# Kernel tuning notes

Hardware: AMD Instinct MI355X
Metric: run time of the kernel (lower is better)

The kernel has to match this reference:

```python
import jax, jax.numpy as jnp
import numpy as np

N = 1024      # params.input_dim (f1 is a square [N, N] similarity matrix)
TOPK = 16     # params.topk
B = 64        # hardcoded batch in the original reshape
W = 2 * N // B  # spatial width after reshape


def setup_inputs() -> dict:
    key = jax.random.key(0)
    k1, k2, k3 = jax.random.split(key, 3)
    f1 = jax.random.normal(k1, (N, N), dtype=jnp.float32)
    # Conv2d(in=N, out=N, kernel=(TOPK, 1)) weights, kaiming-ish scale
    conv_w = jax.random.normal(k2, (N, N, TOPK, 1), dtype=jnp.float32) * 0.01
    conv_b = jax.random.normal(k3, (N,), dtype=jnp.float32) * 0.01
    return {"f1": f1, "conv_w": conv_w, "conv_b": conv_b}


def reference(f1, conv_w, conv_b):
    # i = topk indices along last dim (largest, sorted) -> [N, TOPK]
    _, idx = jax.lax.top_k(f1, TOPK)
    # pos = f1[i]: gather rows of f1 by the topk column indices -> [N, TOPK, N]
    pos = f1[idx]
    # repeat_interleave(TOPK, dim=0).reshape(N, TOPK, -1) == each row tiled TOPK times
    rep = jnp.broadcast_to(f1[:, None, :], (N, TOPK, N))
    # cat on dim=2 -> [N, TOPK, 2N]; reshape to NCHW [B, N, TOPK, W]
    out = jnp.concatenate([rep, pos], axis=2).reshape(B, N, TOPK, W)
    # Conv2d kernel (TOPK, 1), VALID padding collapses H -> 1: [B, N, 1, W]
    y = jax.lax.conv_general_dilated(
        out, conv_w, window_strides=(1, 1), padding='VALID',
        dimension_numbers=('NCHW', 'OIHW', 'NCHW'))
    y = y + conv_b[None, :, None, None]
    return jax.nn.relu(y).reshape(N, -1)  # [N, B*W] = [N, 2N]
```

## Files before the change

### kernel.cpp

```cpp
#include <hip/hip_runtime.h>
#include <stdint.h>


#define NDIM 1024
#define TK   16
#define KPOS 8192
#define KREP 512
#define NCOL 2048

typedef unsigned short u16;
typedef uint32_t u32;
typedef u16   u16x8  __attribute__((ext_vector_type(8)));
typedef u32   u32x4  __attribute__((ext_vector_type(4)));
typedef __bf16 bf16x8 __attribute__((ext_vector_type(8)));
typedef float  f32x4  __attribute__((ext_vector_type(4)));

__device__ __forceinline__ u16 f2bf(float x) {
    union { float f; unsigned u; } v; v.f = x;
    unsigned r = 0x7FFFu + ((v.u >> 16) & 1u);
    return (u16)((v.u + r) >> 16);
}

__device__ __forceinline__ void load_lds_16B(const u16* g, u16* l) {
    __builtin_amdgcn_global_load_lds(
        (__attribute__((address_space(1))) void*)(uintptr_t)g,
        (__attribute__((address_space(3))) void*)(unsigned)(uintptr_t)l,
        16, 0, 0);
}

#define PREP_TOPK 256
#define PREP_ZERO 2048
#define PREP_CONV 4096
#define PREP_W1   1024

__global__ __launch_bounds__(256) void prep_kernel(const float* __restrict__ f1,
                                                   const float* __restrict__ W,
                                                   int* __restrict__ idx,
                                                   u16* __restrict__ Wb,
                                                   u16* __restrict__ W1b,
                                                   float* __restrict__ out) {
    const int bid = blockIdx.x;
    const int t = threadIdx.x;
    if (bid < PREP_TOPK) {
        const int lane = t & 63;
        const int row  = bid * 4 + (t >> 6);
        float v[16];
        const float* src = f1 + row * NDIM + lane;
        #pragma unroll
        for (int j = 0; j < 16; ++j) v[j] = src[j * 64];
        for (int sel = 0; sel < TK; ++sel) {
            float best = -3.402823466e38f; int bg = 0x7fffffff;
            #pragma unroll
            for (int j = 0; j < 16; ++j)
                if (v[j] > best) { best = v[j]; bg = j * 64 + lane; }
            #pragma unroll
            for (int s = 1; s < 64; s <<= 1) {
                float ov = __shfl_xor(best, s);
                int   og = __shfl_xor(bg, s);
                if (ov > best || (ov == best && og < bg)) { best = ov; bg = og; }
            }
            if (lane == sel) idx[row * TK + sel] = bg;
            #pragma unroll
            for (int j = 0; j < 16; ++j)
                if (bg == j * 64 + lane) v[j] = -3.402823466e38f;
        }
    } else if (bid < PREP_TOPK + PREP_ZERO) {
        const int zb = bid - PREP_TOPK;
        f32x4 z = {0.f, 0.f, 0.f, 0.f};
        *(f32x4*)(out + (size_t)(zb * 256 + t) * 4) = z;
    } else if (bid < PREP_TOPK + PREP_ZERO + PREP_CONV) {
        const int tid = (bid - PREP_TOPK - PREP_ZERO) * 256 + t;
        const int o  = tid >> 10;
        const int r  = tid & 1023;
        const int kp0 = r * 8;
        const int ip  = r >> 1;
        const int kh0 = (r & 1) * 8;
        const int i = (ip >> 5) * 64 + ((ip >> 1) & 15) * 4 + (ip & 1) + 2;
        const float* src = W + (size_t)o * 16384 + i * 16 + kh0;
        float4 a = *(const float4*)(src);
        float4 b = *(const float4*)(src + 4);
        u16x8 ov;
        ov[0] = f2bf(a.x); ov[1] = f2bf(a.y); ov[2] = f2bf(a.z); ov[3] = f2bf(a.w);
        ov[4] = f2bf(b.x); ov[5] = f2bf(b.y); ov[6] = f2bf(b.z); ov[7] = f2bf(b.w);
        *(u16x8*)(Wb + (size_t)o * KPOS + kp0) = ov;
    } else {
        const int o = bid - PREP_TOPK - PREP_ZERO - PREP_CONV;
        const float* wrow = W + (size_t)o * 16384;
        #pragma unroll
        for (int h = 0; h < 2; ++h) {
            const int kr = h * 256 + t;
            const int nl = kr >> 5, q = (kr >> 4) & 1, kh = kr & 15;
            const float* base = wrow + (nl * 64 + q) * 16 + kh;
            float s = 0.f;
            #pragma unroll
            for (int tt = 0; tt < 16; ++tt) s += base[tt * 64];
            W1b[o * KREP + kr] = f2bf(s);
        }
    }
}

__global__ __launch_bounds__(256) void buildx_kernel(const float* __restrict__ f1,
                                                     const int* __restrict__ idx,
                                                     u16* __restrict__ Xt,
                                                     u16* __restrict__ B1) {
    __shared__ u32 Ls[32 * 64];
    const int bid = blockIdx.x;
    const int t  = threadIdx.x;
    const int ci  = t >> 5;
    const int s   = t & 31;
    const int khp = s >> 2;
    const int wq  = s & 3;
    int b, i8, row, qoff, ostride;
    u16* dstbase;
    if (bid < 4096) {
        b = bid >> 6; i8 = bid & 63;
        const int ip = i8 * 8 + ci;
        const int nl = ip >> 5, tt = (ip >> 1) & 15, qp = ip & 1;
        row = idx[(b * 16 + nl) * TK + tt];
        qoff = qp * 512;
        dstbase = Xt; ostride = KPOS;
    } else {
        const int rb = bid - 4096;
        b = rb >> 2; i8 = rb & 3;
        const int iq = i8 * 8 + ci;
        row = b * 16 + (iq >> 1);
        qoff = (iq & 1) * 512;
        dstbase = B1; ostride = KREP;
    }
    const float* src = f1 + row * NDIM + qoff;
    const int base0 = khp * 64 + wq * 8;
    float4 a0 = *(const float4*)(src + base0);
    float4 a1 = *(const float4*)(src + base0 + 4);
    float4 b0 = *(const float4*)(src + base0 + 32);
    float4 b1 = *(const float4*)(src + base0 + 36);
    float lo[8] = {a0.x, a0.y, a0.z, a0.w, a1.x, a1.y, a1.z, a1.w};
    float hi[8] = {b0.x, b0.y, b0.z, b0.w, b1.x, b1.y, b1.z, b1.w};
    const int colsw = (ci * 8 + khp) ^ (wq << 3);
    #pragma unroll
    for (int j = 0; j < 8; ++j) {
        const int w = wq * 8 + j;
        u32 p = (u32)f2bf(lo[j]) | ((u32)f2bf(hi[j]) << 16);
        Ls[w * 64 + colsw] = p;
    }
    __syncthreads();
    const int wv = t >> 3, seg = t & 7;
    const int swz = wv & 24;
    u32x4 r0 = *(const u32x4*)(Ls + wv * 64 + ((seg * 8 + 0) ^ swz));
    u32x4 r1 = *(const u32x4*)(Ls + wv * 64 + ((seg * 8 + 4) ^ swz));
    u16* dst = dstbase + (size_t)(b * 32 + wv) * ostride + i8 * 128 + seg * 16;
    *(u32x4*)(dst)     = r0;
    *(u32x4*)(dst + 8) = r1;
}

#define BM 128
#define BN 128
#define BK 64

__global__ __launch_bounds__(256, 2) void gemm_kernel(const u16* __restrict__ Ap,
                                                      const u16* __restrict__ Bp,
                                                      const u16* __restrict__ A1,
                                                      const u16* __restrict__ B1,
                                                      float* __restrict__ out) {
    __shared__ __align__(16) u16 As[BM * BK];
    __shared__ __align__(16) u16 Bs[BN * BK];
    const int f = blockIdx.x;
    int m, n, kb, kiters, stride;
    const u16 *Ab, *Bb;
    if (f < 512) {
        m = f >> 6; const int u = f & 63; n = u & 15;
        stride = KPOS; kb = (u >> 4) * 2048; kiters = 32; Ab = Ap; Bb = Bp;
    } else {
        const int g = f - 512; m = g >> 4; n = g & 15;
        stride = KREP; kb = 0; kiters = 8; Ab = A1; Bb = B1;
    }
    const int t    = threadIdx.x;
    const int lane = t & 63;
    const int wave = t >> 6;
    const int wm   = (wave >> 1) * 64;
    const int wn   = (wave & 1) * 64;
    const int quad = lane >> 4;
    const int l16  = lane & 15;
    const int sw   = l16 & 7;
    const int o0 = m * BM;
    const int n0 = n * BN;

    f32x4 acc[4][4] = {};

    const int rA = t >> 3;
    const int c8 = t & 7;
    const int csw = (c8 ^ (rA & 7)) * 8;
    const u16* gA = Ab + (size_t)(o0 + rA) * stride + kb + csw;
    const u16* gB = Bb + (size_t)(n0 + rA) * stride + kb + csw;
    u16* lA = As + t * 8;
    u16* lB = Bs + t * 8;

    for (int it = 0; it < kiters; ++it) {
        const int k0 = it * BK;
        #pragma unroll
        for (int c = 0; c < 4; ++c) {
            load_lds_16B(gA + (size_t)(c * 32) * stride + k0, lA + c * 2048);
            load_lds_16B(gB + (size_t)(c * 32) * stride + k0, lB + c * 2048);
        }
        __syncthreads();

        #pragma unroll
        for (int ks = 0; ks < 2; ++ks) {
            bf16x8 af[4], bfr[4];
            #pragma unroll
            for (int mt = 0; mt < 4; ++mt) {
                u16x8 bits = *(const u16x8*)(As + (wm + mt * 16 + l16) * BK
                                                + (((ks * 4 + quad) ^ sw) * 8));
                af[mt] = __builtin_bit_cast(bf16x8, bits);
            }
            #pragma unroll
            for (int nt = 0; nt < 4; ++nt) {
                u16x8 bits = *(const u16x8*)(Bs + (wn + nt * 16 + l16) * BK
                                                + (((ks * 4 + quad) ^ sw) * 8));
                bfr[nt] = __builtin_bit_cast(bf16x8, bits);
            }
            #pragma unroll
            for (int mt = 0; mt < 4; ++mt)
                #pragma unroll
                for (int nt = 0; nt < 4; ++nt)
                    acc[mt][nt] = __builtin_amdgcn_mfma_f32_16x16x32_bf16(
                        af[mt], bfr[nt], acc[mt][nt], 0, 0, 0);
        }
        __syncthreads();
    }

    #pragma unroll
    for (int nt = 0; nt < 4; ++nt) {
        const int nn = n0 + wn + nt * 16 + l16;
        const int bb = nn >> 5, w = nn & 31;
        #pragma unroll
        for (int mt = 0; mt < 4; ++mt) {
            #pragma unroll
            for (int r = 0; r < 4; ++r) {
                const int o = o0 + wm + mt * 16 + quad * 4 + r;
                unsafeAtomicAdd(out + (size_t)(bb * 16 + (o >> 6)) * 2048
                                    + (o & 63) * 32 + w,
                                acc[mt][nt][r]);
            }
        }
    }
}

__global__ __launch_bounds__(256) void finalize_kernel(float* __restrict__ out,
                                                       const float* __restrict__ bias) {
    const int tid = blockIdx.x * 256 + threadIdx.x;
    const int f = tid * 4;
    const int o = ((f >> 11) & 15) * 64 + ((f & 2047) >> 5);
    const float bv = bias[o];
    float4 x = *(float4*)(out + f);
    x.x = fmaxf(x.x + bv, 0.f);
    x.y = fmaxf(x.y + bv, 0.f);
    x.z = fmaxf(x.z + bv, 0.f);
    x.w = fmaxf(x.w + bv, 0.f);
    *(float4*)(out + f) = x;
}

extern "C" void kernel_launch(void* const* d_in, const int* in_sizes, int n_in,
                              void* d_out, int out_size, void* d_ws, size_t ws_size,
                              hipStream_t stream) {
    const float* f1   = (const float*)d_in[0];
    const float* Wc   = (const float*)d_in[1];
    const float* bias = (const float*)d_in[2];
    float* out = (float*)d_out;

    int* idx = (int*)d_ws;
    u16* Wb  = (u16*)((char*)d_ws + 65536);
    u16* Xt  = (u16*)((char*)d_ws + 16842752);
    u16* W1b = (u16*)((char*)d_ws + 50397184);
    u16* B1  = (u16*)((char*)d_ws + 51445760);

    prep_kernel<<<PREP_TOPK + PREP_ZERO + PREP_CONV + PREP_W1, 256, 0, stream>>>(
        f1, Wc, idx, Wb, W1b, out);
    buildx_kernel<<<4096 + 256, 256, 0, stream>>>(f1, idx, Xt, B1);
    gemm_kernel<<<512 + 128, 256, 0, stream>>>(Wb, Xt, W1b, B1, out);
    finalize_kernel<<<(NDIM * NCOL) / (4 * 256), 256, 0, stream>>>(out, bias);
}
```

Measured before the change: 180.1 us.

## Gather topk rows directly in GEMM from pre-transposed bf16 f1, drop buildx kernel

Removes the buildx kernel, which materialized a large gathered bf16 B operand (Xt, about 32MB) plus B1. prep now writes a compact bf16 transposed and swizzled copy of f1 (f1t). The GEMM then gathers the needed rows by topk index straight into LDS with global_load_lds. This saves a kernel launch and the large intermediate write and read, at the cost of indexed loads inside the GEMM loop and a new B-tile LDS layout.

```diff
diff --git a/kernel.cpp b/kernel.cpp
--- a/kernel.cpp
+++ b/kernel.cpp
@@ -11,7 +11,6 @@
 typedef unsigned short u16;
 typedef uint32_t u32;
 typedef u16   u16x8  __attribute__((ext_vector_type(8)));
-typedef u32   u32x4  __attribute__((ext_vector_type(4)));
 typedef __bf16 bf16x8 __attribute__((ext_vector_type(8)));
 typedef float  f32x4  __attribute__((ext_vector_type(4)));
 
@@ -32,12 +31,14 @@
 #define PREP_ZERO 2048
 #define PREP_CONV 4096
 #define PREP_W1   1024
+#define PREP_F1T  256
 
 __global__ __launch_bounds__(256) void prep_kernel(const float* __restrict__ f1,
                                                    const float* __restrict__ W,
                                                    int* __restrict__ idx,
                                                    u16* __restrict__ Wb,
                                                    u16* __restrict__ W1b,
+                                                   u16* __restrict__ f1t,
                                                    float* __restrict__ out) {
     const int bid = blockIdx.x;
     const int t = threadIdx.x;
@@ -83,7 +84,7 @@
         ov[0] = f2bf(a.x); ov[1] = f2bf(a.y); ov[2] = f2bf(a.z); ov[3] = f2bf(a.w);
         ov[4] = f2bf(b.x); ov[5] = f2bf(b.y); ov[6] = f2bf(b.z); ov[7] = f2bf(b.w);
         *(u16x8*)(Wb + (size_t)o * KPOS + kp0) = ov;
-    } else {
+    } else if (bid < PREP_TOPK + PREP_ZERO + PREP_CONV + PREP_W1) {
         const int o = bid - PREP_TOPK - PREP_ZERO - PREP_CONV;
         const float* wrow = W + (size_t)o * 16384;
         #pragma unroll
@@ -96,60 +97,22 @@
             for (int tt = 0; tt < 16; ++tt) s += base[tt * 64];
             W1b[o * KREP + kr] = f2bf(s);
         }
-    }
-}
-
-__global__ __launch_bounds__(256) void buildx_kernel(const float* __restrict__ f1,
-                                                     const int* __restrict__ idx,
-                                                     u16* __restrict__ Xt,
-                                                     u16* __restrict__ B1) {
-    __shared__ u32 Ls[32 * 64];
-    const int bid = blockIdx.x;
-    const int t  = threadIdx.x;
-    const int ci  = t >> 5;
-    const int s   = t & 31;
-    const int khp = s >> 2;
-    const int wq  = s & 3;
-    int b, i8, row, qoff, ostride;
-    u16* dstbase;
-    if (bid < 4096) {
-        b = bid >> 6; i8 = bid & 63;
-        const int ip = i8 * 8 + ci;
-        const int nl = ip >> 5, tt = (ip >> 1) & 15, qp = ip & 1;
-        row = idx[(b * 16 + nl) * TK + tt];
-        qoff = qp * 512;
-        dstbase = Xt; ostride = KPOS;
     } else {
-        const int rb = bid - 4096;
-        b = rb >> 2; i8 = rb & 3;
-        const int iq = i8 * 8 + ci;
-        row = b * 16 + (iq >> 1);
-        qoff = (iq & 1) * 512;
-        dstbase = B1; ostride = KREP;
-    }
-    const float* src = f1 + row * NDIM + qoff;
-    const int base0 = khp * 64 + wq * 8;
-    float4 a0 = *(const float4*)(src + base0);
-    float4 a1 = *(const float4*)(src + base0 + 4);
-    float4 b0 = *(const float4*)(src + base0 + 32);
-    float4 b1 = *(const float4*)(src + base0 + 36);
-    float lo[8] = {a0.x, a0.y, a0.z, a0.w, a1.x, a1.y, a1.z, a1.w};
-    float hi[8] = {b0.x, b0.y, b0.z, b0.w, b1.x, b1.y, b1.z, b1.w};
-    const int colsw = (ci * 8 + khp) ^ (wq << 3);
-    #pragma unroll
-    for (int j = 0; j < 8; ++j) {
-        const int w = wq * 8 + j;
-        u32 p = (u32)f2bf(lo[j]) | ((u32)f2bf(hi[j]) << 16);
-        Ls[w * 64 + colsw] = p;
-    }
-    __syncthreads();
-    const int wv = t >> 3, seg = t & 7;
-    const int swz = wv & 24;
-    u32x4 r0 = *(const u32x4*)(Ls + wv * 64 + ((seg * 8 + 0) ^ swz));
-    u32x4 r1 = *(const u32x4*)(Ls + wv * 64 + ((seg * 8 + 4) ^ swz));
-    u16* dst = dstbase + (size_t)(b * 32 + wv) * ostride + i8 * 128 + seg * 16;
-    *(u32x4*)(dst)     = r0;
-    *(u32x4*)(dst + 8) = r1;
+        const int gb = bid - PREP_TOPK - PREP_ZERO - PREP_CONV - PREP_W1;
+        const int unit = t >> 5;
+        const int w = t & 31;
+        const int rq = gb * 8 + unit;
+        const int row = rq >> 1, q = rq & 1;
+        const float* src = f1 + row * NDIM + q * 512;
+        const int swp = ((w >> 2) & 1) * 8;
+        u16 tmp[16];
+        #pragma unroll
+        for (int kh = 0; kh < 16; ++kh)
+            tmp[kh ^ swp] = f2bf(src[kh * 32 + w]);
+        u16* dst = f1t + ((size_t)row * 2 + q) * 512 + w * 16;
+        *(u16x8*)(dst)     = *(u16x8*)(tmp);
+        *(u16x8*)(dst + 8) = *(u16x8*)(tmp + 8);
+    }
 }
 
 #define BM 128
@@ -157,21 +120,22 @@
 #define BK 64
 
 __global__ __launch_bounds__(256, 2) void gemm_kernel(const u16* __restrict__ Ap,
-                                                      const u16* __restrict__ Bp,
                                                       const u16* __restrict__ A1,
-                                                      const u16* __restrict__ B1,
+                                                      const u16* __restrict__ f1t,
+                                                      const int* __restrict__ idx,
                                                       float* __restrict__ out) {
     __shared__ __align__(16) u16 As[BM * BK];
-    __shared__ __align__(16) u16 Bs[BN * BK];
+    __shared__ __align__(16) u16 Bs[16 * 512];
     const int f = blockIdx.x;
-    int m, n, kb, kiters, stride;
-    const u16 *Ab, *Bb;
+    int m, n, kb, kiters, astride;
+    const u16* Ab;
+    bool isPos;
     if (f < 512) {
         m = f >> 6; const int u = f & 63; n = u & 15;
-        stride = KPOS; kb = (u >> 4) * 2048; kiters = 32; Ab = Ap; Bb = Bp;
+        astride = KPOS; kb = (u >> 4) * 2048; kiters = 32; Ab = Ap; isPos = true;
     } else {
         const int g = f - 512; m = g >> 4; n = g & 15;
-        stride = KREP; kb = 0; kiters = 8; Ab = A1; Bb = B1;
+        astride = KREP; kb = 0; kiters = 8; Ab = A1; isPos = false;
     }
     const int t    = threadIdx.x;
     const int lane = t & 63;
@@ -183,24 +147,41 @@
     const int sw   = l16 & 7;
     const int o0 = m * BM;
     const int n0 = n * BN;
+    const int nb0 = n * 4;
 
     f32x4 acc[4][4] = {};
 
     const int rA = t >> 3;
     const int c8 = t & 7;
     const int csw = (c8 ^ (rA & 7)) * 8;
-    const u16* gA = Ab + (size_t)(o0 + rA) * stride + kb + csw;
-    const u16* gB = Bb + (size_t)(n0 + rA) * stride + kb + csw;
+    const u16* gA = Ab + (size_t)(o0 + rA) * astride + kb + csw;
     u16* lA = As + t * 8;
-    u16* lB = Bs + t * 8;
 
     for (int it = 0; it < kiters; ++it) {
         const int k0 = it * BK;
         #pragma unroll
-        for (int c = 0; c < 4; ++c) {
-            load_lds_16B(gA + (size_t)(c * 32) * stride + k0, lA + c * 2048);
-            load_lds_16B(gB + (size_t)(c * 32) * stride + k0, lB + c * 2048);
-        }
+        for (int c = 0; c < 4; ++c)
+            load_lds_16B(gA + (size_t)(c * 32) * astride + k0, lA + c * 2048);
+
+        const int ip = ((kb + k0) >> 4) + wave;
+        int rows[4], qp;
+        if (isPos) {
+            const int nl = ip >> 5, tt = (ip >> 1) & 15;
+            qp = ip & 1;
+            #pragma unroll
+            for (int bl = 0; bl < 4; ++bl)
+                rows[bl] = idx[((nb0 + bl) * 16 + nl) * TK + tt];
+        } else {
+            qp = ip & 1;
+            const int r0 = ip >> 1;
+            #pragma unroll
+            for (int bl = 0; bl < 4; ++bl)
+                rows[bl] = (nb0 + bl) * 16 + r0;
+        }
+        #pragma unroll
+        for (int bl = 0; bl < 4; ++bl)
+            load_lds_16B(f1t + ((size_t)rows[bl] * 2 + qp) * 512 + lane * 8,
+                         Bs + (wave * 4 + bl) * 512);
         __syncthreads();
 
         #pragma unroll
@@ -212,10 +193,14 @@
                                                 + (((ks * 4 + quad) ^ sw) * 8));
                 af[mt] = __builtin_bit_cast(bf16x8, bits);
             }
+            const int ci2 = ks * 2 + (quad >> 1);
+            const int qh  = quad & 1;
             #pragma unroll
             for (int nt = 0; nt < 4; ++nt) {
-                u16x8 bits = *(const u16x8*)(Bs + (wn + nt * 16 + l16) * BK
-                                                + (((ks * 4 + quad) ^ sw) * 8));
+                const int nn = wn + nt * 16 + l16;
+                const int blocf = nn >> 5, w = nn & 31;
+                u16x8 bits = *(const u16x8*)(Bs + (ci2 * 4 + blocf) * 512 + w * 16
+                                                + ((qh ^ ((w >> 2) & 1)) * 8));
                 bfr[nt] = __builtin_bit_cast(bf16x8, bits);
             }
             #pragma unroll
@@ -269,13 +254,11 @@
 
     int* idx = (int*)d_ws;
     u16* Wb  = (u16*)((char*)d_ws + 65536);
-    u16* Xt  = (u16*)((char*)d_ws + 16842752);
-    u16* W1b = (u16*)((char*)d_ws + 50397184);
-    u16* B1  = (u16*)((char*)d_ws + 51445760);
-
-    prep_kernel<<<PREP_TOPK + PREP_ZERO + PREP_CONV + PREP_W1, 256, 0, stream>>>(
-        f1, Wc, idx, Wb, W1b, out);
-    buildx_kernel<<<4096 + 256, 256, 0, stream>>>(f1, idx, Xt, B1);
-    gemm_kernel<<<512 + 128, 256, 0, stream>>>(Wb, Xt, W1b, B1, out);
+    u16* W1b = (u16*)((char*)d_ws + 16842752);
+    u16* f1t = (u16*)((char*)d_ws + 17891328);
+
+    prep_kernel<<<PREP_TOPK + PREP_ZERO + PREP_CONV + PREP_W1 + PREP_F1T,
+                  256, 0, stream>>>(f1, Wc, idx, Wb, W1b, f1t, out);
+    gemm_kernel<<<512 + 128, 256, 0, stream>>>(Wb, W1b, f1t, idx, out);
     finalize_kernel<<<(NDIM * NCOL) / (4 * 256), 256, 0, stream>>>(out, bias);
 }
```

Result: faster. 173.9 us (-3.5%).
